# Kernel tuning notes

Hardware: AMD Instinct MI355X
Metric: run time of the kernel (lower is better)

## Reference

```python
import jax, jax.numpy as jnp
import numpy as np

B, N, NFEAT = 64, 384, 16
E = 3
NHID, NOUT = 128, 128
ST_HID, ST_OUT = 64, 16


def _xavier(key, shape, fan_in, fan_out):
    a = jnp.sqrt(6.0 / (fan_in + fan_out))
    return jax.random.uniform(key, shape, jnp.float32, -a, a)


def setup_inputs() -> dict:
    key = jax.random.key(0)
    ks = jax.random.split(key, 10)
    x = jax.random.normal(ks[0], (B, N, NFEAT), jnp.float32)
    adj = jax.random.uniform(ks[1], (B, E, N, N), jnp.float32)
    emb_w = _xavier(ks[2], (NFEAT, NFEAT), NFEAT, NFEAT)            # Linear(nfeat,nfeat,bias=False)
    gc1_w = _xavier(ks[3], (E, NFEAT, NHID), NFEAT, NHID)           # (edge_dim,in,out)
    gc2_w = _xavier(ks[4], (E, NHID, NHID), NHID, NHID)             # single middle layer (num_layers-2=1)
    gc3_w = _xavier(ks[5], (E, NHID, NOUT), NHID, NOUT)
    st_w1 = _xavier(ks[6], (ST_HID, NOUT), NOUT, ST_HID)            # nn.Linear stores (out,in)
    st_b1 = jnp.zeros((ST_HID,), jnp.float32)
    st_w2 = jnp.full((2 * ST_OUT, ST_HID), 1e-10, jnp.float32)      # init.constant_(linear2.weight, 1e-10)
    st_b2 = jnp.zeros((2 * ST_OUT,), jnp.float32)
    rescale_w = jnp.zeros((1,), jnp.float32)                        # Rescale weight init zero
    return {"x": x, "adj": adj, "emb_w": emb_w, "gc1_w": gc1_w, "gc2_w": gc2_w,
            "gc3_w": gc3_w, "st_w1": st_w1, "st_b1": st_b1, "st_w2": st_w2,
            "st_b2": st_b2, "rescale_w": rescale_w}


def _rgcn_layer(h, adj, W, relu):
    # support: einsum('bid,edh->beih'), aggregate: einsum('beij,bejh->beih'), then sum over e
    support = jnp.einsum('bnd,edh->benh', h, W)
    out = jnp.einsum('bemn,benh->bemh', adj, support)
    if relu:
        out = jax.nn.relu(out)
    return out.sum(axis=1)  # aggregate='sum' over edge types


def reference(x, adj, emb_w, gc1_w, gc2_w, gc3_w, st_w1, st_b1, st_w2, st_b2, rescale_w):
    h = x @ emb_w.T                                   # emb Linear, no bias
    h = _rgcn_layer(h, adj, gc1_w, True)
    h = _rgcn_layer(h, adj, gc2_w, True)
    h = _rgcn_layer(h, adj, gc3_w, False)             # gc3: use_relu=False
    flat = h.reshape(-1, h.shape[-1])                 # (B*N, nout)
    z = jnp.tanh(flat @ st_w1.T + st_b1) @ st_w2.T + st_b2
    s, t = z[:, :ST_OUT], z[:, ST_OUT:]
    s = jnp.exp(rescale_w) * jnp.tanh(s)              # Rescale(tanh(s))
    return jnp.stack([s, t])                          # (2, B*N, ST_OUT)
```

## Files before the change

kernel.cpp:

```cpp
#include <hip/hip_runtime.h>
#include <math.h>

#define ROWS 24576
#define ADJ_BE (384*384)

typedef _Float16 h4v __attribute__((ext_vector_type(4)));
typedef _Float16 h8v __attribute__((ext_vector_type(8)));
typedef float f32x4 __attribute__((ext_vector_type(4)));

#define SPLIT_SCALE 2048.0f
#define INV_SPLIT_SCALE (1.0f / 2048.0f)

__global__ __launch_bounds__(256) void k_h0split(const float* __restrict__ x,
        const float* __restrict__ emb_w, _Float16* __restrict__ Hh, _Float16* __restrict__ Hl) {
    __shared__ float embL[256];
    int t = threadIdx.x;
    if (t < 64) *(float4*)&embL[4 * t] = *(const float4*)(emb_w + 4 * t);
    __syncthreads();
    int gid = blockIdx.x * 256 + t;
    int b = gid / 384, r = gid % 384;
    const float* xp = x + (size_t)gid * 16;
    float xr[16];
    *(float4*)&xr[0]  = *(const float4*)(xp);
    *(float4*)&xr[4]  = *(const float4*)(xp + 4);
    *(float4*)&xr[8]  = *(const float4*)(xp + 8);
    *(float4*)&xr[12] = *(const float4*)(xp + 12);
    size_t base = (size_t)b * 16 * 384 + r;
#pragma unroll
    for (int d = 0; d < 16; ++d) {
        float acc = 0.f;
#pragma unroll
        for (int k = 0; k < 16; ++k) acc = fmaf(xr[k], embL[d * 16 + k], acc);
        _Float16 h = (_Float16)acc;
        Hh[base + (size_t)d * 384] = h;
        Hl[base + (size_t)d * 384] = (_Float16)((acc - (float)h) * SPLIT_SCALE);
    }
}

__global__ __launch_bounds__(256) void k_adj16(const float* __restrict__ adj,
        const _Float16* __restrict__ Hh, const _Float16* __restrict__ Hl,
        float* __restrict__ T1) {
    int mt = blockIdx.x, e = blockIdx.y, b = blockIdx.z;
    const float* A = adj + (size_t)(b * 3 + e) * ADJ_BE + (size_t)mt * 64 * 384;
    const _Float16* BH = Hh + (size_t)b * 16 * 384;
    const _Float16* BL = Hl + (size_t)b * 16 * 384;

    __shared__ _Float16 Af[2][4][4][16][8];

    int t = threadIdx.x;
    int wave = t >> 6, lane = t & 63;
    int l16 = lane & 15, quad = lane >> 4;

    f32x4 acc0 = f32x4{0.f, 0.f, 0.f, 0.f};
    f32x4 acc1 = f32x4{0.f, 0.f, 0.f, 0.f};

    for (int k0 = 0; k0 < 384; k0 += 32) {
        __syncthreads();
#pragma unroll
        for (int p = 0; p < 2; ++p) {
            int idx = t + p * 256;
            int r = idx >> 3, q4 = idx & 7;
            float4 v = *(const float4*)(A + (size_t)r * 384 + k0 + 4 * q4);
            h4v hh, ll;
            float vv[4] = {v.x, v.y, v.z, v.w};
#pragma unroll
            for (int c = 0; c < 4; ++c) {
                _Float16 h = (_Float16)vv[c];
                hh[c] = h;
                ll[c] = (_Float16)((vv[c] - (float)h) * SPLIT_SCALE);
            }
            *(h4v*)&Af[0][r >> 4][q4 >> 1][r & 15][(q4 & 1) * 4] = hh;
            *(h4v*)&Af[1][r >> 4][q4 >> 1][r & 15][(q4 & 1) * 4] = ll;
        }
        h8v b_h = *(const h8v*)(BH + (size_t)l16 * 384 + k0 + 8 * quad);
        h8v b_l = *(const h8v*)(BL + (size_t)l16 * 384 + k0 + 8 * quad);
        __syncthreads();
        h8v a_h = *(const h8v*)&Af[0][wave][quad][l16][0];
        h8v a_l = *(const h8v*)&Af[1][wave][quad][l16][0];
        acc0 = __builtin_amdgcn_mfma_f32_16x16x32_f16(a_h, b_h, acc0, 0, 0, 0);
        acc1 = __builtin_amdgcn_mfma_f32_16x16x32_f16(a_h, b_l, acc1, 0, 0, 0);
        acc1 = __builtin_amdgcn_mfma_f32_16x16x32_f16(a_l, b_h, acc1, 0, 0, 0);
    }
    float* Tp = T1 + ((size_t)(b * 3 + e) * 384 + (size_t)mt * 64 + wave * 16) * 16;
#pragma unroll
    for (int reg = 0; reg < 4; ++reg) {
        float v = fmaf(acc1[reg], INV_SPLIT_SCALE, acc0[reg]);
        Tp[(quad * 4 + reg) * 16 + l16] = v;
    }
}

__global__ __launch_bounds__(256) void k_l1s2(const float* __restrict__ T1,
        const float* __restrict__ W1, float* __restrict__ h1) {
    __shared__ float wL[3][16][128];
    __shared__ float tL[3][64][17];
    int t = threadIdx.x;
    int rt = blockIdx.x;
    int b = rt / 6, m0 = (rt % 6) * 64;
#pragma unroll
    for (int p = 0; p < 6; ++p) {
        int idx = t + p * 256;
        float4 v = *(const float4*)(W1 + (size_t)idx * 4);
        int e = idx / 512, rem = idx % 512;
        int d = rem >> 5, q = rem & 31;
        *(float4*)&wL[e][d][q * 4] = v;
    }
#pragma unroll
    for (int p = 0; p < 3; ++p) {
        int idx = t + p * 256;
        int e = idx >> 8, rem = idx & 255;
        int r = rem >> 2, q = rem & 3;
        float4 v = *(const float4*)(T1 + ((size_t)(b * 3 + e) * 384 + m0 + r) * 16 + q * 4);
        tL[e][r][q*4+0] = v.x; tL[e][r][q*4+1] = v.y; tL[e][r][q*4+2] = v.z; tL[e][r][q*4+3] = v.w;
    }
    __syncthreads();
    int tx = t & 31;
    int ty = t >> 5;
    float tot[8][4] = {};
#pragma unroll
    for (int e = 0; e < 3; ++e) {
        float acc[8][4] = {};
#pragma unroll
        for (int d = 0; d < 16; ++d) {
            float a[8], w[4];
#pragma unroll
            for (int i = 0; i < 8; ++i) a[i] = tL[e][ty + 8 * i][d];
#pragma unroll
            for (int j = 0; j < 4; ++j) w[j] = wL[e][d][tx + 32 * j];
#pragma unroll
            for (int i = 0; i < 8; ++i)
#pragma unroll
                for (int j = 0; j < 4; ++j)
                    acc[i][j] = fmaf(a[i], w[j], acc[i][j]);
        }
#pragma unroll
        for (int i = 0; i < 8; ++i)
#pragma unroll
            for (int j = 0; j < 4; ++j)
                tot[i][j] += fmaxf(acc[i][j], 0.f);
    }
    float* out = h1 + (size_t)rt * 64 * 128;
#pragma unroll
    for (int i = 0; i < 8; ++i)
#pragma unroll
        for (int j = 0; j < 4; ++j)
            out[(ty + 8 * i) * 128 + tx + 32 * j] = tot[i][j];
}

__global__ __launch_bounds__(256) void k_support(const float* __restrict__ hin,
        const float* __restrict__ W, _Float16* __restrict__ Sh, _Float16* __restrict__ Sl) {
    int rt = blockIdx.x, e = blockIdx.y;
    int b = rt / 6, n0 = (rt % 6) * 64;
    const float* Hp = hin + (size_t)rt * 64 * 128;
    const float* Wp = W + (size_t)e * 128 * 128;
    __shared__ float aT[32][68];
    __shared__ float bT[32][132];
    int t = threadIdx.x;
    int tx = t & 15;
    int ty = t >> 4;
    float acc[4][8] = {};
    for (int k0 = 0; k0 < 128; k0 += 32) {
        __syncthreads();
#pragma unroll
        for (int p = 0; p < 2; ++p) {
            int idx = t + p * 256;
            int r = idx >> 3, q = idx & 7;
            float4 v = *(const float4*)(Hp + (size_t)r * 128 + k0 + q * 4);
            aT[q*4+0][r] = v.x; aT[q*4+1][r] = v.y; aT[q*4+2][r] = v.z; aT[q*4+3][r] = v.w;
        }
#pragma unroll
        for (int p = 0; p < 4; ++p) {
            int idx = t + p * 256;
            int r = idx >> 5, q = idx & 31;
            *(float4*)&bT[r][q * 4] = *(const float4*)(Wp + (size_t)(k0 + r) * 128 + q * 4);
        }
        __syncthreads();
#pragma unroll
        for (int k = 0; k < 32; ++k) {
            float4 av = *(const float4*)&aT[k][4 * ty];
            float4 b0 = *(const float4*)&bT[k][4 * tx];
            float4 b1 = *(const float4*)&bT[k][64 + 4 * tx];
            float a[4] = {av.x, av.y, av.z, av.w};
            float bb[8] = {b0.x, b0.y, b0.z, b0.w, b1.x, b1.y, b1.z, b1.w};
#pragma unroll
            for (int i = 0; i < 4; ++i)
#pragma unroll
                for (int j = 0; j < 8; ++j)
                    acc[i][j] = fmaf(a[i], bb[j], acc[i][j]);
        }
    }
    size_t base = (size_t)(b * 3 + e) * 128 * 384;
#pragma unroll
    for (int j = 0; j < 8; ++j) {
        int n = (j < 4) ? (4 * tx + j) : (64 + 4 * tx + j - 4);
        h4v hh, ll;
#pragma unroll
        for (int i = 0; i < 4; ++i) {
            float v = acc[i][j];
            _Float16 h = (_Float16)v;
            hh[i] = h;
            ll[i] = (_Float16)((v - (float)h) * SPLIT_SCALE);
        }
        size_t off = base + (size_t)n * 384 + n0 + 4 * ty;
        *(h4v*)(Sh + off) = hh;
        *(h4v*)(Sl + off) = ll;
    }
}

template <int RELU>
__global__ __launch_bounds__(256, 3) void k_adj_mfma(const float* __restrict__ adj,
        const _Float16* __restrict__ Sh, const _Float16* __restrict__ Sl,
        float* __restrict__ out) {
    int mt = blockIdx.x, e = blockIdx.y, b = blockIdx.z;
    const float* A = adj + (size_t)(b * 3 + e) * ADJ_BE + (size_t)mt * 96 * 384;
    const _Float16* Bh = Sh + (size_t)(b * 3 + e) * 128 * 384;
    const _Float16* Bl = Sl + (size_t)(b * 3 + e) * 128 * 384;
    float* O = out + ((size_t)b * 384 + mt * 96) * 128;

    __shared__ _Float16 Af[2][6][4][16][8];
    __shared__ _Float16 Bf[2][8][4][16][8];

    int t = threadIdx.x;
    int wave = t >> 6, lane = t & 63;
    int l16 = lane & 15, quad = lane >> 4;
    int wm = wave >> 1, wn = wave & 1;

    f32x4 acc0[3][4], acc1[3][4];
#pragma unroll
    for (int i = 0; i < 3; ++i)
#pragma unroll
        for (int j = 0; j < 4; ++j) {
            acc0[i][j] = f32x4{0.f, 0.f, 0.f, 0.f};
            acc1[i][j] = f32x4{0.f, 0.f, 0.f, 0.f};
        }

    for (int k0 = 0; k0 < 384; k0 += 32) {
        __syncthreads();
#pragma unroll
        for (int p = 0; p < 3; ++p) {
            int idx = t + p * 256;
            int r = idx >> 3, q4 = idx & 7;
            float4 v = *(const float4*)(A + (size_t)r * 384 + k0 + 4 * q4);
            h4v hh, ll;
            float vv[4] = {v.x, v.y, v.z, v.w};
#pragma unroll
            for (int c = 0; c < 4; ++c) {
                _Float16 h = (_Float16)vv[c];
                hh[c] = h;
                ll[c] = (_Float16)((vv[c] - (float)h) * SPLIT_SCALE);
            }
            *(h4v*)&Af[0][r >> 4][q4 >> 1][r & 15][(q4 & 1) * 4] = hh;
            *(h4v*)&Af[1][r >> 4][q4 >> 1][r & 15][(q4 & 1) * 4] = ll;
        }
#pragma unroll
        for (int p = 0; p < 2; ++p) {
            int idx = t + p * 256;
            int n = idx >> 2, q8 = idx & 3;
            size_t off = (size_t)n * 384 + k0 + 8 * q8;
            *(h8v*)&Bf[0][n >> 4][q8][n & 15][0] = *(const h8v*)(Bh + off);
            *(h8v*)&Bf[1][n >> 4][q8][n & 15][0] = *(const h8v*)(Bl + off);
        }
        __syncthreads();
        h8v a_h[3], a_l[3];
#pragma unroll
        for (int i = 0; i < 3; ++i) {
            a_h[i] = *(const h8v*)&Af[0][3 * wm + i][quad][l16][0];
            a_l[i] = *(const h8v*)&Af[1][3 * wm + i][quad][l16][0];
        }
#pragma unroll
        for (int j = 0; j < 4; ++j) {
            h8v b_h = *(const h8v*)&Bf[0][4 * wn + j][quad][l16][0];
            h8v b_l = *(const h8v*)&Bf[1][4 * wn + j][quad][l16][0];
#pragma unroll
            for (int i = 0; i < 3; ++i) {
                acc0[i][j] = __builtin_amdgcn_mfma_f32_16x16x32_f16(a_h[i], b_h, acc0[i][j], 0, 0, 0);
                acc1[i][j] = __builtin_amdgcn_mfma_f32_16x16x32_f16(a_h[i], b_l, acc1[i][j], 0, 0, 0);
                acc1[i][j] = __builtin_amdgcn_mfma_f32_16x16x32_f16(a_l[i], b_h, acc1[i][j], 0, 0, 0);
            }
        }
    }
#pragma unroll
    for (int i = 0; i < 3; ++i) {
        int r0 = 48 * wm + 16 * i + quad * 4;
#pragma unroll
        for (int j = 0; j < 4; ++j) {
            int gc = 64 * wn + 16 * j + l16;
#pragma unroll
            for (int reg = 0; reg < 4; ++reg) {
                float v = fmaf(acc1[i][j][reg], INV_SPLIT_SCALE, acc0[i][j][reg]);
                if (RELU) v = fmaxf(v, 0.f);
                atomicAdd(O + (size_t)(r0 + reg) * 128 + gc, v);
            }
        }
    }
}

__global__ void k_zero(float* __restrict__ p, int n4) {
    int i = blockIdx.x * blockDim.x + threadIdx.x;
    if (i < n4) ((float4*)p)[i] = float4{0.f, 0.f, 0.f, 0.f};
}

__global__ __launch_bounds__(256) void k_head(const float* __restrict__ h3,
        const float* __restrict__ st_w1, const float* __restrict__ st_b1,
        const float* __restrict__ st_w2, const float* __restrict__ st_b2,
        const float* __restrict__ rescale_w, float* __restrict__ out) {
    __shared__ float hL[64][132];
    __shared__ float w1L[64][132];
    __shared__ float ytL[64][68];
    __shared__ float w2L[32][68];
    __shared__ float b1L[64], b2L[32];
    int t = threadIdx.x;
    int r0 = blockIdx.x * 64;
#pragma unroll
    for (int p = 0; p < 8; ++p) {
        int idx = t + p * 256;
        int r = idx >> 5, q = idx & 31;
        *(float4*)&hL[r][q * 4] = *(const float4*)(h3 + (size_t)(r0 + r) * 128 + q * 4);
    }
#pragma unroll
    for (int p = 0; p < 8; ++p) {
        int idx = t + p * 256;
        int r = idx >> 5, q = idx & 31;
        *(float4*)&w1L[r][q * 4] = *(const float4*)(st_w1 + (size_t)r * 128 + q * 4);
    }
#pragma unroll
    for (int p = 0; p < 2; ++p) {
        int idx = t + p * 256;
        int r = idx >> 4, q = idx & 15;
        *(float4*)&w2L[r][q * 4] = *(const float4*)(st_w2 + (size_t)r * 64 + q * 4);
    }
    if (t < 64) b1L[t] = st_b1[t];
    else if (t < 96) b2L[t - 64] = st_b2[t - 64];
    __syncthreads();
    int tx = t & 15, ty = t >> 4;
    float acc[4][4] = {};
    for (int d = 0; d < 128; ++d) {
        float a[4], w[4];
#pragma unroll
        for (int i = 0; i < 4; ++i) a[i] = hL[ty + 16 * i][d];
#pragma unroll
        for (int j = 0; j < 4; ++j) w[j] = w1L[tx + 16 * j][d];
#pragma unroll
        for (int i = 0; i < 4; ++i)
#pragma unroll
            for (int j = 0; j < 4; ++j)
                acc[i][j] = fmaf(a[i], w[j], acc[i][j]);
    }
#pragma unroll
    for (int i = 0; i < 4; ++i)
#pragma unroll
        for (int j = 0; j < 4; ++j)
            ytL[ty + 16 * i][tx + 16 * j] = tanhf(acc[i][j] + b1L[tx + 16 * j]);
    __syncthreads();
    int tx8 = t & 7, ty32 = t >> 3;
    float acc2[2][4] = {};
    for (int d = 0; d < 64; ++d) {
        float a[2], w[4];
#pragma unroll
        for (int i = 0; i < 2; ++i) a[i] = ytL[ty32 + 32 * i][d];
#pragma unroll
        for (int j = 0; j < 4; ++j) w[j] = w2L[tx8 + 8 * j][d];
#pragma unroll
        for (int i = 0; i < 2; ++i)
#pragma unroll
            for (int j = 0; j < 4; ++j)
                acc2[i][j] = fmaf(a[i], w[j], acc2[i][j]);
    }
    float er = expf(rescale_w[0]);
#pragma unroll
    for (int i = 0; i < 2; ++i) {
        int r = r0 + ty32 + 32 * i;
#pragma unroll
        for (int j = 0; j < 4; ++j) {
            int c = tx8 + 8 * j;
            float z = acc2[i][j] + b2L[c];
            if (c < 16) out[(size_t)r * 16 + c] = er * tanhf(z);
            else        out[(size_t)(ROWS + r) * 16 + (c - 16)] = z;
        }
    }
}

extern "C" void kernel_launch(void* const* d_in, const int* in_sizes, int n_in,
                              void* d_out, int out_size, void* d_ws, size_t ws_size,
                              hipStream_t stream) {
    const float* x     = (const float*)d_in[0];
    const float* adj   = (const float*)d_in[1];
    const float* emb_w = (const float*)d_in[2];
    const float* gc1   = (const float*)d_in[3];
    const float* gc2   = (const float*)d_in[4];
    const float* gc3   = (const float*)d_in[5];
    const float* st_w1 = (const float*)d_in[6];
    const float* st_b1 = (const float*)d_in[7];
    const float* st_w2 = (const float*)d_in[8];
    const float* st_b2 = (const float*)d_in[9];
    const float* resc  = (const float*)d_in[10];
    float* out = (float*)d_out;
    float* ws  = (float*)d_ws;

    float* T1 = ws;
    float* hA = T1 + 1179648;
    float* hB = hA + 3145728;
    _Float16* Sh = (_Float16*)(hB + 3145728);
    _Float16* Sl = Sh + 9437184;
    _Float16* Hh = (_Float16*)hB;
    _Float16* Hl = Hh + 393216;

    k_h0split<<<96, 256, 0, stream>>>(x, emb_w, Hh, Hl);
    k_adj16<<<dim3(6, 3, 64), 256, 0, stream>>>(adj, Hh, Hl, T1);
    k_l1s2<<<384, 256, 0, stream>>>(T1, gc1, hA);
    k_support<<<dim3(384, 3), 256, 0, stream>>>(hA, gc2, Sh, Sl);
    k_zero<<<3072, 256, 0, stream>>>(hB, 786432);
    k_adj_mfma<1><<<dim3(4, 3, 64), 256, 0, stream>>>(adj, Sh, Sl, hB);
    k_support<<<dim3(384, 3), 256, 0, stream>>>(hB, gc3, Sh, Sl);
    k_zero<<<3072, 256, 0, stream>>>(hA, 786432);
    k_adj_mfma<0><<<dim3(4, 3, 64), 256, 0, stream>>>(adj, Sh, Sl, hA);
    k_head<<<384, 256, 0, stream>>>(hA, st_w1, st_b1, st_w2, st_b2, resc, out);
}
```

Baseline: 441.3 us.

## Register-prefetch next adjacency and support tiles; shrink adj MFMA row tile to 64

Both adjacency GEMM kernels now load the next K-slice of adjacency (and support/H tiles) into registers while the MFMAs for the current slice run, hiding global load latency behind compute. k_adj_mfma also drops its M tile from 96 to 64 rows, giving a 6x3x64 grid with more blocks and fewer accumulator registers. The cost is more registers for prefetch buffers, an extra barrier per iteration, and re-reading the support matrix for more row tiles.

```diff
diff --git a/kernel.cpp b/kernel.cpp
--- a/kernel.cpp
+++ b/kernel.cpp
@@ -50,36 +50,50 @@
     int t = threadIdx.x;
     int wave = t >> 6, lane = t & 63;
     int l16 = lane & 15, quad = lane >> 4;
+    int r0s = t >> 3, q4s = t & 7;
 
     f32x4 acc0 = f32x4{0.f, 0.f, 0.f, 0.f};
     f32x4 acc1 = f32x4{0.f, 0.f, 0.f, 0.f};
 
-    for (int k0 = 0; k0 < 384; k0 += 32) {
-        __syncthreads();
+    float4 ra[2];
+    h8v rbh, rbl;
+#pragma unroll
+    for (int p = 0; p < 2; ++p)
+        ra[p] = *(const float4*)(A + (size_t)(r0s + 32 * p) * 384 + 4 * q4s);
+    rbh = *(const h8v*)(BH + (size_t)l16 * 384 + 8 * quad);
+    rbl = *(const h8v*)(BL + (size_t)l16 * 384 + 8 * quad);
+
+    for (int kc = 0; kc < 12; ++kc) {
 #pragma unroll
         for (int p = 0; p < 2; ++p) {
-            int idx = t + p * 256;
-            int r = idx >> 3, q4 = idx & 7;
-            float4 v = *(const float4*)(A + (size_t)r * 384 + k0 + 4 * q4);
+            int r = r0s + 32 * p;
+            float vv[4] = {ra[p].x, ra[p].y, ra[p].z, ra[p].w};
             h4v hh, ll;
-            float vv[4] = {v.x, v.y, v.z, v.w};
 #pragma unroll
             for (int c = 0; c < 4; ++c) {
                 _Float16 h = (_Float16)vv[c];
                 hh[c] = h;
                 ll[c] = (_Float16)((vv[c] - (float)h) * SPLIT_SCALE);
             }
-            *(h4v*)&Af[0][r >> 4][q4 >> 1][r & 15][(q4 & 1) * 4] = hh;
-            *(h4v*)&Af[1][r >> 4][q4 >> 1][r & 15][(q4 & 1) * 4] = ll;
-        }
-        h8v b_h = *(const h8v*)(BH + (size_t)l16 * 384 + k0 + 8 * quad);
-        h8v b_l = *(const h8v*)(BL + (size_t)l16 * 384 + k0 + 8 * quad);
-        __syncthreads();
+            *(h4v*)&Af[0][r >> 4][q4s >> 1][r & 15][(q4s & 1) * 4] = hh;
+            *(h4v*)&Af[1][r >> 4][q4s >> 1][r & 15][(q4s & 1) * 4] = ll;
+        }
+        h8v b_h = rbh, b_l = rbl;
+        __syncthreads();
+        if (kc + 1 < 12) {
+            int kn = (kc + 1) * 32;
+#pragma unroll
+            for (int p = 0; p < 2; ++p)
+                ra[p] = *(const float4*)(A + (size_t)(r0s + 32 * p) * 384 + kn + 4 * q4s);
+            rbh = *(const h8v*)(BH + (size_t)l16 * 384 + kn + 8 * quad);
+            rbl = *(const h8v*)(BL + (size_t)l16 * 384 + kn + 8 * quad);
+        }
         h8v a_h = *(const h8v*)&Af[0][wave][quad][l16][0];
         h8v a_l = *(const h8v*)&Af[1][wave][quad][l16][0];
         acc0 = __builtin_amdgcn_mfma_f32_16x16x32_f16(a_h, b_h, acc0, 0, 0, 0);
         acc1 = __builtin_amdgcn_mfma_f32_16x16x32_f16(a_h, b_l, acc1, 0, 0, 0);
         acc1 = __builtin_amdgcn_mfma_f32_16x16x32_f16(a_l, b_h, acc1, 0, 0, 0);
+        __syncthreads();
     }
     float* Tp = T1 + ((size_t)(b * 3 + e) * 384 + (size_t)mt * 64 + wave * 16) * 16;
 #pragma unroll
@@ -211,76 +225,100 @@
         const _Float16* __restrict__ Sh, const _Float16* __restrict__ Sl,
         float* __restrict__ out) {
     int mt = blockIdx.x, e = blockIdx.y, b = blockIdx.z;
-    const float* A = adj + (size_t)(b * 3 + e) * ADJ_BE + (size_t)mt * 96 * 384;
+    const float* A = adj + (size_t)(b * 3 + e) * ADJ_BE + (size_t)mt * 64 * 384;
     const _Float16* Bh = Sh + (size_t)(b * 3 + e) * 128 * 384;
     const _Float16* Bl = Sl + (size_t)(b * 3 + e) * 128 * 384;
-    float* O = out + ((size_t)b * 384 + mt * 96) * 128;
-
-    __shared__ _Float16 Af[2][6][4][16][8];
+    float* O = out + ((size_t)b * 384 + mt * 64) * 128;
+
+    __shared__ _Float16 Af[2][4][4][16][8];
     __shared__ _Float16 Bf[2][8][4][16][8];
 
     int t = threadIdx.x;
     int wave = t >> 6, lane = t & 63;
     int l16 = lane & 15, quad = lane >> 4;
     int wm = wave >> 1, wn = wave & 1;
-
-    f32x4 acc0[3][4], acc1[3][4];
-#pragma unroll
-    for (int i = 0; i < 3; ++i)
+    int r0s = t >> 3, q4s = t & 7;
+    int nB = t >> 2, q8B = t & 3;
+
+    f32x4 acc0[2][4], acc1[2][4];
+#pragma unroll
+    for (int i = 0; i < 2; ++i)
 #pragma unroll
         for (int j = 0; j < 4; ++j) {
             acc0[i][j] = f32x4{0.f, 0.f, 0.f, 0.f};
             acc1[i][j] = f32x4{0.f, 0.f, 0.f, 0.f};
         }
 
+    float4 ra[2];
+    h8v rb[4];
+#pragma unroll
+    for (int p = 0; p < 2; ++p)
+        ra[p] = *(const float4*)(A + (size_t)(r0s + 32 * p) * 384 + 4 * q4s);
+#pragma unroll
+    for (int p = 0; p < 4; ++p) {
+        int si = t + 256 * (p & 1);
+        int n = si >> 2, q8 = si & 3;
+        const _Float16* Bsrc = (p < 2) ? Bh : Bl;
+        rb[p] = *(const h8v*)(Bsrc + (size_t)n * 384 + 8 * q8);
+    }
+
     for (int k0 = 0; k0 < 384; k0 += 32) {
-        __syncthreads();
-#pragma unroll
-        for (int p = 0; p < 3; ++p) {
-            int idx = t + p * 256;
-            int r = idx >> 3, q4 = idx & 7;
-            float4 v = *(const float4*)(A + (size_t)r * 384 + k0 + 4 * q4);
+#pragma unroll
+        for (int p = 0; p < 2; ++p) {
+            int r = r0s + 32 * p;
+            float vv[4] = {ra[p].x, ra[p].y, ra[p].z, ra[p].w};
             h4v hh, ll;
-            float vv[4] = {v.x, v.y, v.z, v.w};
 #pragma unroll
             for (int c = 0; c < 4; ++c) {
                 _Float16 h = (_Float16)vv[c];
                 hh[c] = h;
                 ll[c] = (_Float16)((vv[c] - (float)h) * SPLIT_SCALE);
             }
-            *(h4v*)&Af[0][r >> 4][q4 >> 1][r & 15][(q4 & 1) * 4] = hh;
-            *(h4v*)&Af[1][r >> 4][q4 >> 1][r & 15][(q4 & 1) * 4] = ll;
-        }
-#pragma unroll
-        for (int p = 0; p < 2; ++p) {
-            int idx = t + p * 256;
-            int n = idx >> 2, q8 = idx & 3;
-            size_t off = (size_t)n * 384 + k0 + 8 * q8;
-            *(h8v*)&Bf[0][n >> 4][q8][n & 15][0] = *(const h8v*)(Bh + off);
-            *(h8v*)&Bf[1][n >> 4][q8][n & 15][0] = *(const h8v*)(Bl + off);
-        }
-        __syncthreads();
-        h8v a_h[3], a_l[3];
-#pragma unroll
-        for (int i = 0; i < 3; ++i) {
-            a_h[i] = *(const h8v*)&Af[0][3 * wm + i][quad][l16][0];
-            a_l[i] = *(const h8v*)&Af[1][3 * wm + i][quad][l16][0];
+            *(h4v*)&Af[0][r >> 4][q4s >> 1][r & 15][(q4s & 1) * 4] = hh;
+            *(h4v*)&Af[1][r >> 4][q4s >> 1][r & 15][(q4s & 1) * 4] = ll;
+        }
+#pragma unroll
+        for (int p = 0; p < 4; ++p) {
+            int si = t + 256 * (p & 1);
+            int n = si >> 2, q8 = si & 3;
+            *(h8v*)&Bf[p >> 1][n >> 4][q8][n & 15][0] = rb[p];
+        }
+        __syncthreads();
+        if (k0 + 32 < 384) {
+            int kn = k0 + 32;
+#pragma unroll
+            for (int p = 0; p < 2; ++p)
+                ra[p] = *(const float4*)(A + (size_t)(r0s + 32 * p) * 384 + kn + 4 * q4s);
+#pragma unroll
+            for (int p = 0; p < 4; ++p) {
+                int si = t + 256 * (p & 1);
+                int n = si >> 2, q8 = si & 3;
+                const _Float16* Bsrc = (p < 2) ? Bh : Bl;
+                rb[p] = *(const h8v*)(Bsrc + (size_t)n * 384 + kn + 8 * q8);
+            }
+        }
+        h8v a_h[2], a_l[2];
+#pragma unroll
+        for (int i = 0; i < 2; ++i) {
+            a_h[i] = *(const h8v*)&Af[0][2 * wm + i][quad][l16][0];
+            a_l[i] = *(const h8v*)&Af[1][2 * wm + i][quad][l16][0];
         }
 #pragma unroll
         for (int j = 0; j < 4; ++j) {
             h8v b_h = *(const h8v*)&Bf[0][4 * wn + j][quad][l16][0];
             h8v b_l = *(const h8v*)&Bf[1][4 * wn + j][quad][l16][0];
 #pragma unroll
-            for (int i = 0; i < 3; ++i) {
+            for (int i = 0; i < 2; ++i) {
                 acc0[i][j] = __builtin_amdgcn_mfma_f32_16x16x32_f16(a_h[i], b_h, acc0[i][j], 0, 0, 0);
                 acc1[i][j] = __builtin_amdgcn_mfma_f32_16x16x32_f16(a_h[i], b_l, acc1[i][j], 0, 0, 0);
                 acc1[i][j] = __builtin_amdgcn_mfma_f32_16x16x32_f16(a_l[i], b_h, acc1[i][j], 0, 0, 0);
             }
         }
-    }
-#pragma unroll
-    for (int i = 0; i < 3; ++i) {
-        int r0 = 48 * wm + 16 * i + quad * 4;
+        __syncthreads();
+    }
+#pragma unroll
+    for (int i = 0; i < 2; ++i) {
+        int r0 = 32 * wm + 16 * i + quad * 4;
 #pragma unroll
         for (int j = 0; j < 4; ++j) {
             int gc = 64 * wn + 16 * j + l16;
@@ -409,9 +447,9 @@
     k_l1s2<<<384, 256, 0, stream>>>(T1, gc1, hA);
     k_support<<<dim3(384, 3), 256, 0, stream>>>(hA, gc2, Sh, Sl);
     k_zero<<<3072, 256, 0, stream>>>(hB, 786432);
-    k_adj_mfma<1><<<dim3(4, 3, 64), 256, 0, stream>>>(adj, Sh, Sl, hB);
+    k_adj_mfma<1><<<dim3(6, 3, 64), 256, 0, stream>>>(adj, Sh, Sl, hB);
     k_support<<<dim3(384, 3), 256, 0, stream>>>(hB, gc3, Sh, Sl);
     k_zero<<<3072, 256, 0, stream>>>(hA, 786432);
-    k_adj_mfma<0><<<dim3(4, 3, 64), 256, 0, stream>>>(adj, Sh, Sl, hA);
+    k_adj_mfma<0><<<dim3(6, 3, 64), 256, 0, stream>>>(adj, Sh, Sl, hA);
     k_head<<<384, 256, 0, stream>>>(hA, st_w1, st_b1, st_w2, st_b2, resc, out);
 }
```

Measured after the change: 451.5 us. +2.3%, slower.
